# Performance work log

Measured on AMD Instinct MI355X. Metric: run time of the kernel, lower is better.

The kernel has to match this reference:

```python
import jax, jax.numpy as jnp
import numpy as np
import math

D_MODEL = 512
N_HEADS = 8
FACTOR = 5
B, L_Q, L_K = 8, 4096, 4096


def setup_inputs() -> dict:
    key = jax.random.key(0)
    ks = jax.random.split(key, 9)
    s = 0.02
    sample_k = max(1, int(FACTOR * math.log(L_K + 1)))  # 41
    return {
        "query": jax.random.normal(ks[0], (B, L_Q, D_MODEL), jnp.float32),
        "key_in": jax.random.normal(ks[1], (B, L_K, D_MODEL), jnp.float32),
        "value": jax.random.normal(ks[2], (B, L_K, D_MODEL), jnp.float32),
        "W_Q": jax.random.normal(ks[3], (D_MODEL, D_MODEL), jnp.float32) * s,
        "W_K": jax.random.normal(ks[4], (D_MODEL, D_MODEL), jnp.float32) * s,
        "W_V": jax.random.normal(ks[5], (D_MODEL, D_MODEL), jnp.float32) * s,
        "W_out": jax.random.normal(ks[6], (D_MODEL, D_MODEL), jnp.float32) * s,
        "b_out": jnp.zeros((D_MODEL,), jnp.float32),
        "sample_idx": jax.random.randint(ks[8], (L_Q, sample_k), 0, L_K),
    }


def reference(query, key_in, value, W_Q, W_K, W_V, W_out, b_out, sample_idx):
    b, lq, _ = query.shape
    lk = key_in.shape[1]
    H = N_HEADS
    E = D_MODEL // H
    # projections -> [B, H, L, E]
    Q = (query @ W_Q).reshape(b, lq, H, E).transpose(0, 2, 1, 3)
    K = (key_in @ W_K).reshape(b, lk, H, E).transpose(0, 2, 1, 3)
    V = (value @ W_V).reshape(b, lk, H, E).transpose(0, 2, 1, 3)

    u = max(1, int(FACTOR * math.log(lq + 1)))  # top-u queries (41)

    # sparsity proxy M(q_i, K) on randomly sampled keys
    K_sample = K[:, :, sample_idx, :]                      # [B,H,L_Q,S,E]
    QK_sample = jnp.einsum('bhqe,bhqse->bhqs', Q, K_sample)
    M = QK_sample.max(axis=-1) - QK_sample.mean(axis=-1)   # [B,H,L_Q]
    _, M_top = jax.lax.top_k(M, u)                         # [B,H,u]

    # attention for the top-u queries only
    Q_reduce = jnp.take_along_axis(Q, M_top[..., None], axis=2)  # [B,H,u,E]
    scale = 1.0 / math.sqrt(E)
    scores = jnp.einsum('bhue,bhke->bhuk', Q_reduce, K) * scale
    attn = jax.nn.softmax(scores, axis=-1)  # dropout is identity (eval)
    ctx_top = jnp.einsum('bhuk,bhke->bhue', attn, V)       # [B,H,u,E]

    # mean-value context for the lazy queries, scatter-update the active ones
    ctx = jnp.broadcast_to(V.mean(axis=2, keepdims=True), (b, H, lq, E))
    bi = jnp.arange(b)[:, None, None]
    hi = jnp.arange(H)[None, :, None]
    ctx = ctx.at[bi, hi, M_top].set(ctx_top)

    ctx = ctx.transpose(0, 2, 1, 3).reshape(b, lq, H * E)
    return ctx @ W_out + b_out
```

## Files before the change

kernel.cpp:

```cpp
#include <hip/hip_runtime.h>
#include <cstdint>
#include <cstddef>

#define D_MODEL 512
#define NHEADS  8
#define EDIM    64
#define BATCH   8
#define LSEQ    4096

typedef unsigned short u16;
typedef __attribute__((ext_vector_type(8))) short short8;
typedef __attribute__((ext_vector_type(4))) float f32x4;

__device__ __forceinline__ u16 bf16_rne(float x) {
  unsigned int u = __float_as_uint(x);
  u += 0x7FFFu + ((u >> 16) & 1u);
  return (u16)(u >> 16);
}
__device__ __forceinline__ void split2(float x, u16& h, u16& l) {
  h = bf16_rne(x);
  float hf = __uint_as_float((unsigned int)h << 16);
  l = bf16_rne(x - hf);
}

__global__ __launch_bounds__(256) void cvt_x(
    const float* __restrict__ X, u16* __restrict__ P, int planeStride) {
  size_t i = ((size_t)blockIdx.x * 256 + threadIdx.x) * 4;
  float4 x = *(const float4*)(X + i);
  ushort4 h, l;
  split2(x.x, h.x, l.x);
  split2(x.y, h.y, l.y);
  split2(x.z, h.z, l.z);
  split2(x.w, h.w, l.w);
  *(ushort4*)(P + i) = h;
  *(ushort4*)(P + planeStride + i) = l;
}

__global__ __launch_bounds__(256) void cvt_w(
    const float* __restrict__ W0, const float* __restrict__ W1,
    const float* __restrict__ W2, u16* __restrict__ out) {
  const float* W = (blockIdx.z == 0) ? W0 : ((blockIdx.z == 1) ? W1 : W2);
  u16* P = out + (size_t)blockIdx.z * 524288;
  __shared__ float tile[64][65];
  const int k0 = blockIdx.x * 64, n0 = blockIdx.y * 64;
  const int t = threadIdx.x;
  const int tr = t >> 4, tc = (t & 15) * 4;
#pragma unroll
  for (int j = 0; j < 4; ++j) {
    int kr = tr + j * 16;
    float4 v = *(const float4*)(W + (size_t)(k0 + kr) * 512 + n0 + tc);
    tile[kr][tc + 0] = v.x; tile[kr][tc + 1] = v.y;
    tile[kr][tc + 2] = v.z; tile[kr][tc + 3] = v.w;
  }
  __syncthreads();
#pragma unroll
  for (int j = 0; j < 4; ++j) {
    int nr = tr + j * 16;
    ushort4 h, l;
    split2(tile[tc + 0][nr], h.x, l.x);
    split2(tile[tc + 1][nr], h.y, l.y);
    split2(tile[tc + 2][nr], h.z, l.z);
    split2(tile[tc + 3][nr], h.w, l.w);
    size_t off = (size_t)(n0 + nr) * 512 + k0 + tc;
    *(ushort4*)(P + off) = h;
    *(ushort4*)(P + 262144 + off) = l;
  }
}

__device__ __forceinline__ void gld_lds16(const char* g, char* l) {
  __builtin_amdgcn_global_load_lds((const __attribute__((address_space(1))) void*)g,
                                   (__attribute__((address_space(3))) void*)l, 16, 0, 0);
}

__global__ __launch_bounds__(256, 2) void gemm_mfma(
    const u16* __restrict__ XP, int xPlaneStride,
    const u16* __restrict__ WP, float* __restrict__ Y) {
  __shared__ u16 Ah[128 * 32];
  __shared__ u16 Al[128 * 32];
  __shared__ u16 Bh[128 * 32];
  __shared__ u16 Bl[128 * 32];
  const int tid = threadIdx.x;
  const int lane = tid & 63, wv = tid >> 6;
  const int wm = (wv & 1) * 64, wn = (wv >> 1) * 64;
  const int bm = blockIdx.x * 128, bn = blockIdx.y * 128;
  const int fr = lane & 15, quad = lane >> 4;
  const int sRow = tid >> 2, sColB = (tid & 3) * 16;

  f32x4 acc[16];
#pragma unroll
  for (int i = 0; i < 16; ++i) acc[i] = (f32x4){0.f, 0.f, 0.f, 0.f};

  const u16* Xh = XP;
  const u16* Xl = XP + xPlaneStride;
  const u16* Wh = WP;
  const u16* Wl = WP + 262144;

  for (int kk = 0; kk < 16; ++kk) {
#pragma unroll
    for (int j = 0; j < 2; ++j) {
      const size_t rA = (size_t)(bm + j * 64 + sRow) * 512 + kk * 32;
      const size_t rB = (size_t)(bn + j * 64 + sRow) * 512 + kk * 32;
      const int lo = (j * 256 + wv * 64) * 16;
      gld_lds16((const char*)(Xh + rA) + sColB, (char*)Ah + lo);
      gld_lds16((const char*)(Xl + rA) + sColB, (char*)Al + lo);
      gld_lds16((const char*)(Wh + rB) + sColB, (char*)Bh + lo);
      gld_lds16((const char*)(Wl + rB) + sColB, (char*)Bl + lo);
    }
    __syncthreads();
    short8 ah[4], al[4], bh[4], bl[4];
#pragma unroll
    for (int mi = 0; mi < 4; ++mi) {
      ah[mi] = *(const short8*)&Ah[(wm + mi * 16 + fr) * 32 + quad * 8];
      al[mi] = *(const short8*)&Al[(wm + mi * 16 + fr) * 32 + quad * 8];
    }
#pragma unroll
    for (int ni = 0; ni < 4; ++ni) {
      bh[ni] = *(const short8*)&Bh[(wn + ni * 16 + fr) * 32 + quad * 8];
      bl[ni] = *(const short8*)&Bl[(wn + ni * 16 + fr) * 32 + quad * 8];
    }
#pragma unroll
    for (int mi = 0; mi < 4; ++mi)
#pragma unroll
      for (int ni = 0; ni < 4; ++ni)
        acc[mi * 4 + ni] = __builtin_amdgcn_mfma_f32_16x16x32_bf16(
            ah[mi], bh[ni], acc[mi * 4 + ni], 0, 0, 0);
#pragma unroll
    for (int mi = 0; mi < 4; ++mi)
#pragma unroll
      for (int ni = 0; ni < 4; ++ni)
        acc[mi * 4 + ni] = __builtin_amdgcn_mfma_f32_16x16x32_bf16(
            ah[mi], bl[ni], acc[mi * 4 + ni], 0, 0, 0);
#pragma unroll
    for (int mi = 0; mi < 4; ++mi)
#pragma unroll
      for (int ni = 0; ni < 4; ++ni)
        acc[mi * 4 + ni] = __builtin_amdgcn_mfma_f32_16x16x32_bf16(
            al[mi], bh[ni], acc[mi * 4 + ni], 0, 0, 0);
    __syncthreads();
  }
#pragma unroll
  for (int mi = 0; mi < 4; ++mi)
#pragma unroll
    for (int ni = 0; ni < 4; ++ni) {
      const f32x4 a = acc[mi * 4 + ni];
      float* yp = Y + (size_t)(bm + wm + mi * 16 + quad * 4) * 512 + (bn + wn + ni * 16 + fr);
#pragma unroll
      for (int r = 0; r < 4; ++r) yp[(size_t)r * 512] = a[r];
    }
}

__global__ __launch_bounds__(256) void qk_sample_half(
    const float* __restrict__ Q, const float* __restrict__ K,
    const int* __restrict__ sidx, float* __restrict__ M, int S, int hg) {
  const int blk = blockIdx.x;
  const int lane = threadIdx.x & 63;
  const int b = blk & 7;
  const int q = ((blk >> 3) << 2) + (threadIdx.x >> 6);
  const int s = lane >> 5;
  const int hl = (lane >> 3) & 3;
  const int d = lane & 7;
  const int h = hg * 4 + hl;
  const int col = hg * 256 + hl * 64 + d * 8;

  const float* Qp = Q + ((size_t)b * LSEQ + q) * D_MODEL + col;
  const float4 q0 = *(const float4*)Qp;
  const float4 q1 = *(const float4*)(Qp + 4);
  const float* Kb = K + (size_t)b * LSEQ * D_MODEL + col;
  const int* sp = sidx + (size_t)q * S;

  auto rowp = [&](int j) -> const float* {
    int jj = j + s;
    int row = sp[(jj < S) ? jj : (S - 1)];
    return Kb + (size_t)row * D_MODEL;
  };

  const float* pr0 = rowp(0);
  float4 a0 = *(const float4*)pr0, b0 = *(const float4*)(pr0 + 4);
  const float* pr1 = rowp(2);
  float4 a1 = *(const float4*)pr1, b1 = *(const float4*)(pr1 + 4);

  float mx = -3.4e38f, sum = 0.0f;
  for (int j = 0; j < S; j += 2) {
    const float4 ca = a0, cb = b0;
    a0 = a1; b0 = b1;
    const float* pn = rowp(j + 4);
    a1 = *(const float4*)pn;
    b1 = *(const float4*)(pn + 4);
    float p = ca.x * q0.x + ca.y * q0.y + ca.z * q0.z + ca.w * q0.w +
              cb.x * q1.x + cb.y * q1.y + cb.z * q1.z + cb.w * q1.w;
    p += __shfl_xor(p, 1, 64);
    p += __shfl_xor(p, 2, 64);
    p += __shfl_xor(p, 4, 64);
    if (j + s < S) {
      mx = fmaxf(mx, p);
      sum += p;
    }
  }
  mx = fmaxf(mx, __shfl_xor(mx, 32, 64));
  sum += __shfl_xor(sum, 32, 64);
  if (s == 0 && d == 0)
    M[((size_t)(b * NHEADS + h)) * LSEQ + q] = mx - sum / (float)S;
}

__global__ __launch_bounds__(256) void topk_kernel(
    const float* __restrict__ M, int* __restrict__ Mtop, int U) {
  __shared__ float vals[LSEQ];
  __shared__ float rmax[256];
  __shared__ int ridx[256];
  int bh = blockIdx.x;
  int t = threadIdx.x;
  for (int i = t; i < LSEQ; i += 256) vals[i] = M[(size_t)bh * LSEQ + i];
  __syncthreads();
  for (int it = 0; it < U; ++it) {
    float best = -3.4e38f; int bi = -1;
    for (int i = t; i < LSEQ; i += 256) {
      float v = vals[i];
      if (v > best) { best = v; bi = i; }
    }
    rmax[t] = best; ridx[t] = bi;
    __syncthreads();
    for (int s = 128; s > 0; s >>= 1) {
      if (t < s) {
        if (rmax[t + s] > rmax[t]) { rmax[t] = rmax[t + s]; ridx[t] = ridx[t + s]; }
      }
      __syncthreads();
    }
    if (t == 0) {
      Mtop[(size_t)bh * U + it] = ridx[0];
      vals[ridx[0]] = -3.4e38f;
    }
    __syncthreads();
  }
}

__global__ __launch_bounds__(256, 2) void attn_flash(
    const float* __restrict__ Q, const float* __restrict__ K,
    const float* __restrict__ V, const int* __restrict__ Mtop,
    float* __restrict__ part_ctx, float* __restrict__ part_m,
    float* __restrict__ part_l, int U, int nsplit, int chunks_per_block) {
  __shared__ u16 KhS[64 * 72];
  __shared__ u16 KlS[64 * 72];
  __shared__ float VsS[64 * 68];
  const int bh = blockIdx.y, split = blockIdx.x;
  const int h = bh & (NHEADS - 1), b = bh >> 3;
  const int t = threadIdx.x, w = t >> 6, lane = t & 63;
  const int fr = lane & 15, quad = lane >> 4;

  const int qi = w * 16 + fr;
  const int qrow = (qi < U) ? Mtop[(size_t)bh * U + qi] : Mtop[(size_t)bh * U];
  const float4* Qr = (const float4*)(Q + ((size_t)(b * LSEQ) + qrow) * D_MODEL + h * EDIM);
  float4 qa = Qr[quad * 2], qb = Qr[quad * 2 + 1];
  float4 qc = Qr[quad * 2 + 8], qd = Qr[quad * 2 + 9];
  short8 qh0, ql0, qh1, ql1;
  {
    u16 hh, ll;
    split2(qa.x, hh, ll); qh0[0] = (short)hh; ql0[0] = (short)ll;
    split2(qa.y, hh, ll); qh0[1] = (short)hh; ql0[1] = (short)ll;
    split2(qa.z, hh, ll); qh0[2] = (short)hh; ql0[2] = (short)ll;
    split2(qa.w, hh, ll); qh0[3] = (short)hh; ql0[3] = (short)ll;
    split2(qb.x, hh, ll); qh0[4] = (short)hh; ql0[4] = (short)ll;
    split2(qb.y, hh, ll); qh0[5] = (short)hh; ql0[5] = (short)ll;
    split2(qb.z, hh, ll); qh0[6] = (short)hh; ql0[6] = (short)ll;
    split2(qb.w, hh, ll); qh0[7] = (short)hh; ql0[7] = (short)ll;
    split2(qc.x, hh, ll); qh1[0] = (short)hh; ql1[0] = (short)ll;
    split2(qc.y, hh, ll); qh1[1] = (short)hh; ql1[1] = (short)ll;
    split2(qc.z, hh, ll); qh1[2] = (short)hh; ql1[2] = (short)ll;
    split2(qc.w, hh, ll); qh1[3] = (short)hh; ql1[3] = (short)ll;
    split2(qd.x, hh, ll); qh1[4] = (short)hh; ql1[4] = (short)ll;
    split2(qd.y, hh, ll); qh1[5] = (short)hh; ql1[5] = (short)ll;
    split2(qd.z, hh, ll); qh1[6] = (short)hh; ql1[6] = (short)ll;
    split2(qd.w, hh, ll); qh1[7] = (short)hh; ql1[7] = (short)ll;
  }

  float4 c4[16];
#pragma unroll
  for (int i = 0; i < 16; ++i) c4[i] = make_float4(0.f, 0.f, 0.f, 0.f);
  float m = -1e30f, l = 0.0f;

  const int r = t >> 2, cg = t & 3;

  const int k_base = split * (chunks_per_block * 64);
  for (int c = 0; c < chunks_per_block; ++c) {
    const int k0 = k_base + c * 64;
    const float4* Kg4 = (const float4*)(K + ((size_t)(b * LSEQ) + k0 + r) * D_MODEL + h * EDIM);
    const float4* Vg4 = (const float4*)(V + ((size_t)(b * LSEQ) + k0 + r) * D_MODEL + h * EDIM);
#pragma unroll
    for (int i = 0; i < 4; ++i) {
      const int f4 = cg + 4 * i;
      float4 kv = Kg4[f4];
      float4 vv = Vg4[f4];
      ushort4 hh, ll;
      split2(kv.x, hh.x, ll.x);
      split2(kv.y, hh.y, ll.y);
      split2(kv.z, hh.z, ll.z);
      split2(kv.w, hh.w, ll.w);
      *(ushort4*)&KhS[r * 72 + f4 * 4] = hh;
      *(ushort4*)&KlS[r * 72 + f4 * 4] = ll;
      *(float4*)&VsS[r * 68 + f4 * 4] = vv;
    }
    __syncthreads();

    f32x4 acc[4];
#pragma unroll
    for (int mt = 0; mt < 4; ++mt) acc[mt] = (f32x4){0.f, 0.f, 0.f, 0.f};
#pragma unroll
    for (int mt = 0; mt < 4; ++mt) {
      short8 kh = *(const short8*)&KhS[(mt * 16 + fr) * 72 + quad * 8];
      short8 kl = *(const short8*)&KlS[(mt * 16 + fr) * 72 + quad * 8];
      acc[mt] = __builtin_amdgcn_mfma_f32_16x16x32_bf16(kh, qh0, acc[mt], 0, 0, 0);
      acc[mt] = __builtin_amdgcn_mfma_f32_16x16x32_bf16(kh, ql0, acc[mt], 0, 0, 0);
      acc[mt] = __builtin_amdgcn_mfma_f32_16x16x32_bf16(kl, qh0, acc[mt], 0, 0, 0);
    }
#pragma unroll
    for (int mt = 0; mt < 4; ++mt) {
      short8 kh = *(const short8*)&KhS[(mt * 16 + fr) * 72 + 32 + quad * 8];
      short8 kl = *(const short8*)&KlS[(mt * 16 + fr) * 72 + 32 + quad * 8];
      acc[mt] = __builtin_amdgcn_mfma_f32_16x16x32_bf16(kh, qh1, acc[mt], 0, 0, 0);
      acc[mt] = __builtin_amdgcn_mfma_f32_16x16x32_bf16(kh, ql1, acc[mt], 0, 0, 0);
      acc[mt] = __builtin_amdgcn_mfma_f32_16x16x32_bf16(kl, qh1, acc[mt], 0, 0, 0);
    }

    float cm = -3.4e38f;
#pragma unroll
    for (int mt = 0; mt < 4; ++mt) {
#pragma unroll
      for (int rr = 0; rr < 4; ++rr) {
        float s = acc[mt][rr] * 0.125f;
        acc[mt][rr] = s;
        cm = fmaxf(cm, s);
      }
    }
    cm = fmaxf(cm, __shfl_xor(cm, 16, 64));
    cm = fmaxf(cm, __shfl_xor(cm, 32, 64));
    float mn = fmaxf(m, cm);
    if (mn > m) {
      float f = __expf(m - mn);
      l *= f;
#pragma unroll
      for (int i = 0; i < 16; ++i) {
        c4[i].x *= f; c4[i].y *= f; c4[i].z *= f; c4[i].w *= f;
      }
      m = mn;
    }
    float psum = 0.0f;
#pragma unroll
    for (int mt = 0; mt < 4; ++mt) {
#pragma unroll
      for (int rr = 0; rr < 4; ++rr) {
        float p = __expf(acc[mt][rr] - m);
        acc[mt][rr] = p;
        psum += p;
      }
    }
    l += psum;

#pragma unroll
    for (int mt = 0; mt < 4; ++mt) {
#pragma unroll
      for (int rr = 0; rr < 4; ++rr) {
        const int krow = mt * 16 + quad * 4 + rr;
        const float4* vr = (const float4*)&VsS[krow * 68];
        const float p = acc[mt][rr];
#pragma unroll
        for (int i = 0; i < 16; ++i) {
          float4 vv = vr[i];
          c4[i].x += p * vv.x; c4[i].y += p * vv.y;
          c4[i].z += p * vv.z; c4[i].w += p * vv.w;
        }
      }
    }
    __syncthreads();
  }

#pragma unroll
  for (int i = 0; i < 16; ++i) {
    c4[i].x += __shfl_xor(c4[i].x, 16, 64);
    c4[i].y += __shfl_xor(c4[i].y, 16, 64);
    c4[i].z += __shfl_xor(c4[i].z, 16, 64);
    c4[i].w += __shfl_xor(c4[i].w, 16, 64);
    c4[i].x += __shfl_xor(c4[i].x, 32, 64);
    c4[i].y += __shfl_xor(c4[i].y, 32, 64);
    c4[i].z += __shfl_xor(c4[i].z, 32, 64);
    c4[i].w += __shfl_xor(c4[i].w, 32, 64);
  }
  l += __shfl_xor(l, 16, 64);
  l += __shfl_xor(l, 32, 64);

  if (quad == 0 && qi < U) {
    part_m[(size_t)(bh * nsplit + split) * 64 + qi] = m;
    part_l[(size_t)(bh * nsplit + split) * 64 + qi] = l;
  }
  float* pc = part_ctx + (size_t)(bh * nsplit + split) * 4096;
  if (quad == 0) {
#pragma unroll
    for (int ii = 0; ii < 16; ++ii) pc[ii * 64 + qi] = (&c4[ii >> 2].x)[ii & 3];
  } else if (quad == 1) {
#pragma unroll
    for (int ii = 0; ii < 16; ++ii) pc[(16 + ii) * 64 + qi] = (&c4[4 + (ii >> 2)].x)[ii & 3];
  } else if (quad == 2) {
#pragma unroll
    for (int ii = 0; ii < 16; ++ii) pc[(32 + ii) * 64 + qi] = (&c4[8 + (ii >> 2)].x)[ii & 3];
  } else {
#pragma unroll
    for (int ii = 0; ii < 16; ++ii) pc[(48 + ii) * 64 + qi] = (&c4[12 + (ii >> 2)].x)[ii & 3];
  }
}

__global__ __launch_bounds__(256) void attn_combine(
    const float* __restrict__ part_ctx, const float* __restrict__ part_m,
    const float* __restrict__ part_l, float* __restrict__ ctxTop,
    int U, int nsplit) {
  __shared__ float F[16][64];
  const int bh = blockIdx.x;
  const int t = threadIdx.x, lane = t & 63, grp = t >> 6;
  if (grp == 0) {
    float M = -3.4e38f;
    for (int s = 0; s < nsplit; ++s)
      M = fmaxf(M, part_m[(size_t)(bh * nsplit + s) * 64 + lane]);
    float L = 0.0f;
    for (int s = 0; s < nsplit; ++s)
      L += part_l[(size_t)(bh * nsplit + s) * 64 + lane] *
           __expf(part_m[(size_t)(bh * nsplit + s) * 64 + lane] - M);
    float invL = 1.0f / L;
    for (int s = 0; s < nsplit; ++s)
      F[s][lane] = __expf(part_m[(size_t)(bh * nsplit + s) * 64 + lane] - M) * invL;
  }
  __syncthreads();
  for (int ei = 0; ei < 16; ++ei) {
    int e = grp * 16 + ei;
    float acc = 0.0f;
    for (int s = 0; s < nsplit; ++s)
      acc += F[s][lane] * part_ctx[(size_t)(bh * nsplit + s) * 4096 + e * 64 + lane];
    if (lane < U) ctxTop[((size_t)bh * U + lane) * 64 + e] = acc;
  }
}

__global__ __launch_bounds__(256) void vmean_kernel(
    const float* __restrict__ V, float* __restrict__ Vm) {
  __shared__ float part[4][EDIM];
  int bh = blockIdx.x;
  int h = bh & (NHEADS - 1), b = bh >> 3;
  int t = threadIdx.x;
  int e = t & 63, c = t >> 6;
  float s = 0.0f;
  for (int k = c * (LSEQ / 4); k < (c + 1) * (LSEQ / 4); ++k)
    s += V[((size_t)b * LSEQ + k) * D_MODEL + h * EDIM + e];
  part[c][e] = s;
  __syncthreads();
  if (c == 0)
    Vm[(size_t)bh * EDIM + e] =
        (part[0][e] + part[1][e] + part[2][e] + part[3][e]) * (1.0f / (float)LSEQ);
}

__global__ __launch_bounds__(256) void base_out_kernel(
    const float* __restrict__ Vm, const float* __restrict__ Wout,
    const float* __restrict__ bout, float* __restrict__ base) {
  __shared__ float cb[D_MODEL];
  int b = blockIdx.x;
  int t = threadIdx.x;
  for (int d = t; d < D_MODEL; d += 256) cb[d] = Vm[(size_t)b * D_MODEL + d];
  __syncthreads();
  for (int n = t; n < D_MODEL; n += 256) {
    float s = bout[n];
    for (int d = 0; d < D_MODEL; ++d) s += cb[d] * Wout[(size_t)d * D_MODEL + n];
    base[(size_t)b * D_MODEL + n] = s;
  }
}

__global__ __launch_bounds__(256) void fill_out(
    const float* __restrict__ base, float* __restrict__ out) {
  size_t i = (size_t)blockIdx.x * 256 + threadIdx.x;
  int n4 = (int)(i & 127);
  size_t bq = i >> 7;
  int b = (int)(bq >> 12);
  float4 v = ((const float4*)base)[(size_t)b * 128 + n4];
  ((float4*)out)[i] = v;
}

__global__ __launch_bounds__(256) void delta_out(
    const float* __restrict__ ctxTop, const float* __restrict__ Vm,
    const int* __restrict__ Mtop, const float* __restrict__ Wout,
    float* __restrict__ out, int U) {
  __shared__ float dlt[EDIM];
  int blk = blockIdx.x;
  int u = blk % U, bh = blk / U;
  int h = bh & (NHEADS - 1), b = bh >> 3;
  int q = Mtop[(size_t)bh * U + u];
  int t = threadIdx.x;
  if (t < EDIM)
    dlt[t] = ctxTop[((size_t)bh * U + u) * EDIM + t] - Vm[(size_t)bh * EDIM + t];
  __syncthreads();
  float* orow = out + ((size_t)b * LSEQ + q) * D_MODEL;
  for (int n = t; n < D_MODEL; n += 256) {
    float s = 0.0f;
#pragma unroll
    for (int e = 0; e < EDIM; ++e) s += dlt[e] * Wout[(size_t)(h * EDIM + e) * D_MODEL + n];
    atomicAdd(&orow[n], s);
  }
}

extern "C" void kernel_launch(void* const* d_in, const int* in_sizes, int n_in,
                              void* d_out, int out_size, void* d_ws, size_t ws_size,
                              hipStream_t stream) {
  const float* query  = (const float*)d_in[0];
  const float* key_in = (const float*)d_in[1];
  const float* value  = (const float*)d_in[2];
  const float* W_Q    = (const float*)d_in[3];
  const float* W_K    = (const float*)d_in[4];
  const float* W_V    = (const float*)d_in[5];
  const float* W_out  = (const float*)d_in[6];
  const float* b_out  = (const float*)d_in[7];
  const int*   sidx   = (const int*)d_in[8];
  float* out = (float*)d_out;

  const int S = in_sizes[8] / LSEQ;
  const int U = S;

  char* ws = (char*)d_ws;
  size_t o = 0;
  float* Qf     = (float*)(ws + o); o += (size_t)BATCH * LSEQ * D_MODEL * 4;
  float* Kf     = (float*)(ws + o); o += (size_t)BATCH * LSEQ * D_MODEL * 4;
  float* Vf     = (float*)(ws + o); o += (size_t)BATCH * LSEQ * D_MODEL * 4;
  int*   Mtop   = (int*)  (ws + o); o += ((size_t)64 * U * 4 + 255) & ~255ULL;
  float* ctxTop = (float*)(ws + o); o += ((size_t)64 * U * EDIM * 4 + 255) & ~255ULL;
  float* Vm     = (float*)(ws + o); o += 16384;
  float* baseO  = (float*)(ws + o); o += 16384;
  u16*   Wpl    = (u16*)  (ws + o); o += (size_t)3 * 524288 * 2;
  size_t unionOff = o;

  int nchunk = 1;
  while (nchunk < 16 &&
         unionOff + 2 * ((size_t)(32768 / nchunk) * 512 * 2) > ws_size)
    nchunk <<= 1;
  const int Mchunk = 32768 / nchunk;
  u16* planes = (u16*)(ws + unionOff);
  const int planeStride = Mchunk * 512;

  float* M = (float*)(ws + unionOff);
  int nsplit = 16;
  for (;;) {
    size_t need = unionOff + 2 * ((size_t)64 * nsplit * 64 * 4)
                  + (size_t)64 * nsplit * 4096 * 4;
    if (need <= ws_size || nsplit == 1) break;
    nsplit >>= 1;
  }
  float* part_m   = (float*)(ws + unionOff);
  float* part_l   = part_m + (size_t)64 * nsplit * 64;
  float* part_ctx = part_l + (size_t)64 * nsplit * 64;
  const int chunks_per_block = 64 / nsplit;

  cvt_w<<<dim3(8, 8, 3), 256, 0, stream>>>(W_Q, W_K, W_V, Wpl);
  const float* Xsrc[3] = {query, key_in, value};
  float* Ydst[3] = {Qf, Kf, Vf};
  for (int g = 0; g < 3; ++g) {
    for (int c = 0; c < nchunk; ++c) {
      const float* xc = Xsrc[g] + (size_t)c * Mchunk * 512;
      float* yc = Ydst[g] + (size_t)c * Mchunk * 512;
      cvt_x<<<(Mchunk * 512) / 1024, 256, 0, stream>>>(xc, planes, planeStride);
      gemm_mfma<<<dim3(Mchunk / 128, 4), 256, 0, stream>>>(
          planes, planeStride, Wpl + (size_t)g * 524288, yc);
    }
  }

  qk_sample_half<<<(BATCH * LSEQ) / 4, 256, 0, stream>>>(Qf, Kf, sidx, M, S, 0);
  qk_sample_half<<<(BATCH * LSEQ) / 4, 256, 0, stream>>>(Qf, Kf, sidx, M, S, 1);
  topk_kernel<<<BATCH * NHEADS, 256, 0, stream>>>(M, Mtop, U);
  attn_flash<<<dim3(nsplit, BATCH * NHEADS), 256, 0, stream>>>(
      Qf, Kf, Vf, Mtop, part_ctx, part_m, part_l, U, nsplit, chunks_per_block);
  attn_combine<<<BATCH * NHEADS, 256, 0, stream>>>(
      part_ctx, part_m, part_l, ctxTop, U, nsplit);
  vmean_kernel<<<BATCH * NHEADS, 256, 0, stream>>>(Vf, Vm);
  base_out_kernel<<<BATCH, 256, 0, stream>>>(Vm, W_out, b_out, baseO);
  fill_out<<<(BATCH * LSEQ * (D_MODEL / 4)) / 256, 256, 0, stream>>>(baseO, out);
  delta_out<<<BATCH * NHEADS * U, 256, 0, stream>>>(ctxTop, Vm, Mtop, W_out, out, U);
}
```

Before: 918.6 us.

## Compute top-u output delta with split-bf16 MFMA per batch-head block

Replaces the per-query scalar delta_out kernel (one block per selected query) with an MFMA kernel that handles all selected queries of a batch-head in one block. W_out is converted to hi/lo bf16 planes alongside the other weights, and the deltas are split into hi/lo bf16 for three-pass MFMA to keep near-fp32 accuracy. The aim is to cut redundant W_out reads and scalar FMA work. The cost is a larger weight-conversion launch, only 64 blocks of work, and a limit of at most 64 selected queries per block.

Result: faster. 843.0 us (-8.2%).

```diff
diff --git a/kernel.cpp b/kernel.cpp
--- a/kernel.cpp
+++ b/kernel.cpp
@@ -38,8 +38,10 @@
 
 __global__ __launch_bounds__(256) void cvt_w(
     const float* __restrict__ W0, const float* __restrict__ W1,
-    const float* __restrict__ W2, u16* __restrict__ out) {
-  const float* W = (blockIdx.z == 0) ? W0 : ((blockIdx.z == 1) ? W1 : W2);
+    const float* __restrict__ W2, const float* __restrict__ W3,
+    u16* __restrict__ out) {
+  const float* W = (blockIdx.z == 0) ? W0 : ((blockIdx.z == 1) ? W1 :
+                   ((blockIdx.z == 2) ? W2 : W3));
   u16* P = out + (size_t)blockIdx.z * 524288;
   __shared__ float tile[64][65];
   const int k0 = blockIdx.x * 64, n0 = blockIdx.y * 64;
@@ -477,26 +479,91 @@
   ((float4*)out)[i] = v;
 }
 
-__global__ __launch_bounds__(256) void delta_out(
+__global__ __launch_bounds__(256, 1) void delta_out_mfma(
     const float* __restrict__ ctxTop, const float* __restrict__ Vm,
-    const int* __restrict__ Mtop, const float* __restrict__ Wout,
+    const int* __restrict__ Mtop, const u16* __restrict__ WoutTP,
     float* __restrict__ out, int U) {
-  __shared__ float dlt[EDIM];
-  int blk = blockIdx.x;
-  int u = blk % U, bh = blk / U;
-  int h = bh & (NHEADS - 1), b = bh >> 3;
-  int q = Mtop[(size_t)bh * U + u];
-  int t = threadIdx.x;
-  if (t < EDIM)
-    dlt[t] = ctxTop[((size_t)bh * U + u) * EDIM + t] - Vm[(size_t)bh * EDIM + t];
+  __shared__ u16 Dh[64 * 72];
+  __shared__ u16 Dl[64 * 72];
+  __shared__ int qr[64];
+  const int bh = blockIdx.x;
+  const int h = bh & (NHEADS - 1), b = bh >> 3;
+  const int t = threadIdx.x, lane = t & 63, wv = t >> 6;
+  const int fr = lane & 15, quad = lane >> 4;
+
+  {
+    const int r = t >> 2, c0 = (t & 3) * 16;
+#pragma unroll
+    for (int j = 0; j < 4; ++j) {
+      float4 v = make_float4(0.f, 0.f, 0.f, 0.f);
+      if (r < U) {
+        float4 cv = *(const float4*)(ctxTop + ((size_t)bh * U + r) * EDIM + c0 + j * 4);
+        float4 mv = *(const float4*)(Vm + (size_t)bh * EDIM + c0 + j * 4);
+        v = make_float4(cv.x - mv.x, cv.y - mv.y, cv.z - mv.z, cv.w - mv.w);
+      }
+      ushort4 hh, ll;
+      split2(v.x, hh.x, ll.x);
+      split2(v.y, hh.y, ll.y);
+      split2(v.z, hh.z, ll.z);
+      split2(v.w, hh.w, ll.w);
+      *(ushort4*)&Dh[r * 72 + c0 + j * 4] = hh;
+      *(ushort4*)&Dl[r * 72 + c0 + j * 4] = ll;
+    }
+  }
+  if (t < 64) qr[t] = (t < U) ? Mtop[(size_t)bh * U + t] : -1;
   __syncthreads();
-  float* orow = out + ((size_t)b * LSEQ + q) * D_MODEL;
-  for (int n = t; n < D_MODEL; n += 256) {
-    float s = 0.0f;
-#pragma unroll
-    for (int e = 0; e < EDIM; ++e) s += dlt[e] * Wout[(size_t)(h * EDIM + e) * D_MODEL + n];
-    atomicAdd(&orow[n], s);
-  }
+
+  f32x4 acc[32];
+#pragma unroll
+  for (int i = 0; i < 32; ++i) acc[i] = (f32x4){0.f, 0.f, 0.f, 0.f};
+
+  const u16* Wh = WoutTP;
+  const u16* Wl = WoutTP + 262144;
+
+#pragma unroll
+  for (int ks = 0; ks < 2; ++ks) {
+    short8 a_h[4], a_l[4];
+#pragma unroll
+    for (int mt = 0; mt < 4; ++mt) {
+      a_h[mt] = *(const short8*)&Dh[(mt * 16 + fr) * 72 + ks * 32 + quad * 8];
+      a_l[mt] = *(const short8*)&Dl[(mt * 16 + fr) * 72 + ks * 32 + quad * 8];
+    }
+#pragma unroll
+    for (int nt = 0; nt < 8; ++nt) {
+      const int n = wv * 128 + nt * 16 + fr;
+      const size_t off = (size_t)n * 512 + h * EDIM + ks * 32 + quad * 8;
+      short8 b_h = *(const short8*)&Wh[off];
+      short8 b_l = *(const short8*)&Wl[off];
+#pragma unroll
+      for (int mt = 0; mt < 4; ++mt) {
+        acc[mt * 8 + nt] = __builtin_amdgcn_mfma_f32_16x16x32_bf16(
+            a_h[mt], b_h, acc[mt * 8 + nt], 0, 0, 0);
+        acc[mt * 8 + nt] = __builtin_amdgcn_mfma_f32_16x16x32_bf16(
+            a_h[mt], b_l, acc[mt * 8 + nt], 0, 0, 0);
+        acc[mt * 8 + nt] = __builtin_amdgcn_mfma_f32_16x16x32_bf16(
+            a_l[mt], b_h, acc[mt * 8 + nt], 0, 0, 0);
+      }
+    }
+  }
+
+  int qreg[16];
+#pragma unroll
+  for (int mt = 0; mt < 4; ++mt)
+#pragma unroll
+    for (int r4 = 0; r4 < 4; ++r4) qreg[mt * 4 + r4] = qr[mt * 16 + quad * 4 + r4];
+#pragma unroll
+  for (int mt = 0; mt < 4; ++mt)
+#pragma unroll
+    for (int nt = 0; nt < 8; ++nt) {
+      const f32x4 a = acc[mt * 8 + nt];
+      const int n = wv * 128 + nt * 16 + fr;
+#pragma unroll
+      for (int r4 = 0; r4 < 4; ++r4) {
+        const int q = qreg[mt * 4 + r4];
+        if (q >= 0)
+          atomicAdd(out + ((size_t)b * LSEQ + q) * D_MODEL + n, a[r4]);
+      }
+    }
 }
 
 extern "C" void kernel_launch(void* const* d_in, const int* in_sizes, int n_in,
@@ -525,7 +592,7 @@
   float* ctxTop = (float*)(ws + o); o += ((size_t)64 * U * EDIM * 4 + 255) & ~255ULL;
   float* Vm     = (float*)(ws + o); o += 16384;
   float* baseO  = (float*)(ws + o); o += 16384;
-  u16*   Wpl    = (u16*)  (ws + o); o += (size_t)3 * 524288 * 2;
+  u16*   Wpl    = (u16*)  (ws + o); o += (size_t)4 * 524288 * 2;
   size_t unionOff = o;
 
   int nchunk = 1;
@@ -549,7 +616,7 @@
   float* part_ctx = part_l + (size_t)64 * nsplit * 64;
   const int chunks_per_block = 64 / nsplit;
 
-  cvt_w<<<dim3(8, 8, 3), 256, 0, stream>>>(W_Q, W_K, W_V, Wpl);
+  cvt_w<<<dim3(8, 8, 4), 256, 0, stream>>>(W_Q, W_K, W_V, W_out, Wpl);
   const float* Xsrc[3] = {query, key_in, value};
   float* Ydst[3] = {Qf, Kf, Vf};
   for (int g = 0; g < 3; ++g) {
@@ -572,5 +639,6 @@
   vmean_kernel<<<BATCH * NHEADS, 256, 0, stream>>>(Vf, Vm);
   base_out_kernel<<<BATCH, 256, 0, stream>>>(Vm, W_out, b_out, baseO);
   fill_out<<<(BATCH * LSEQ * (D_MODEL / 4)) / 256, 256, 0, stream>>>(baseO, out);
-  delta_out<<<BATCH * NHEADS * U, 256, 0, stream>>>(ctxTop, Vm, Mtop, W_out, out, U);
-}
+  delta_out_mfma<<<BATCH * NHEADS, 256, 0, stream>>>(
+      ctxTop, Vm, Mtop, Wpl + (size_t)3 * 524288, out, U);
+}
```
